# Kernel tuning notes

Measured on AMD Instinct MI355X. Metric: run time of the kernel, lower is better.

The kernel has to match this reference:

```python
import jax, jax.numpy as jnp
import numpy as np

B, Q, HID = 2, 2048, 2048
HQ, HKV, D = 16, 4, 128
EPS = 1e-6
THETA = 1000000.0


def _rmsnorm(x, w):
    # x: [..., D]
    return x * jax.lax.rsqrt(jnp.mean(x * x, axis=-1, keepdims=True) + EPS) * w


def _rope(x, cos, sin):
    # neox-style: split halves. x: [B,Q,H,D], cos/sin: [B,Q,1,D/2]
    d2 = x.shape[-1] // 2
    x1, x2 = x[..., :d2], x[..., d2:]
    return jnp.concatenate([x1 * cos - x2 * sin, x2 * cos + x1 * sin], axis=-1)


def setup_inputs() -> dict:
    key = jax.random.key(0)
    k1, k2, k3 = jax.random.split(key, 3)
    positions = jnp.broadcast_to(jnp.arange(Q, dtype=jnp.int32), (B, Q))
    hidden_states = jax.random.normal(k1, (B, Q, HID), dtype=jnp.float32)
    k_cache = jnp.zeros((B, HKV, Q, D), dtype=jnp.float32)
    v_cache = jnp.zeros((B, HKV, Q, D), dtype=jnp.float32)
    wqkv = jax.random.normal(k2, (HQ * D + 2 * HKV * D, HID), dtype=jnp.float32) * (HID ** -0.5)
    wo = jax.random.normal(k3, (HID, HQ * D), dtype=jnp.float32) * ((HQ * D) ** -0.5)
    q_norm_w = jnp.ones((D,), dtype=jnp.float32)
    k_norm_w = jnp.ones((D,), dtype=jnp.float32)
    return {"positions": positions, "hidden_states": hidden_states, "k_cache": k_cache,
            "v_cache": v_cache, "wqkv": wqkv, "wo": wo, "q_norm_w": q_norm_w,
            "k_norm_w": k_norm_w, "seq_len": Q}


def reference(positions, hidden_states, k_cache, v_cache, wqkv, wo, q_norm_w, k_norm_w, seq_len):
    bsz, qlen, _ = hidden_states.shape
    q_size, kv_size = HQ * D, HKV * D
    scale = D ** -0.5

    qkv = hidden_states.reshape(bsz * qlen, HID) @ wqkv.T  # [B*Q, q+2kv]
    q = qkv[:, :q_size].reshape(bsz, qlen, HQ, D)
    k = qkv[:, q_size:q_size + kv_size].reshape(bsz, qlen, HKV, D)
    v = qkv[:, q_size + kv_size:].reshape(bsz, qlen, HKV, D)

    q = _rmsnorm(q, q_norm_w)
    k = _rmsnorm(k, k_norm_w)

    inv_freq = 1.0 / (THETA ** (jnp.arange(0, D, 2, dtype=jnp.float32) / D))  # [D/2]
    freqs = positions.astype(jnp.float32)[..., None] * inv_freq  # [B,Q,D/2]
    cos = jnp.cos(freqs)[:, :, None, :]
    sin = jnp.sin(freqs)[:, :, None, :]
    q = _rope(q, cos, sin)
    k = _rope(k, cos, sin)

    q = q.transpose(0, 2, 1, 3)  # [B,HQ,Q,D]
    k = k.transpose(0, 2, 1, 3)  # [B,HKV,Q,D]
    v = v.transpose(0, 2, 1, 3)

    start = seq_len - qlen
    k_cache = jax.lax.dynamic_update_slice(k_cache, k, (0, 0, start, 0))
    v_cache = jax.lax.dynamic_update_slice(v_cache, v, (0, 0, start, 0))
    k_full = k_cache[:, :, :seq_len, :]
    v_full = v_cache[:, :, :seq_len, :]

    rep = HQ // HKV
    kf = jnp.repeat(k_full, rep, axis=1)  # [B,HQ,S,D]
    vf = jnp.repeat(v_full, rep, axis=1)

    scores = jnp.einsum('bhqd,bhkd->bhqk', q, kf) * scale
    if qlen == seq_len:  # is_causal path
        causal = jnp.tril(jnp.ones((qlen, seq_len), dtype=bool))
        scores = jnp.where(causal, scores, jnp.finfo(scores.dtype).min)
    attn = jax.nn.softmax(scores, axis=-1)
    out = jnp.einsum('bhqk,bhkd->bhqd', attn, vf)  # [B,HQ,Q,D]
    out = out.transpose(0, 2, 1, 3).reshape(bsz * qlen, HQ * D)
    return (out @ wo.T).reshape(bsz, qlen, HID)
```

## Files before the change

kernel.cpp:

```cpp
#include <hip/hip_runtime.h>

#define B_    2
#define Q_    2048
#define HID_  2048
#define HQ_   16
#define HKV_  4
#define D_    128
#define QSC_  (0.08838834764831843f * 1.4426950408889634f)
#define LOG2_THETA 19.931568569324174f
#define FMAX_ 20.0f

typedef unsigned short u16;
typedef __attribute__((ext_vector_type(8))) short bf16x8;
typedef __attribute__((ext_vector_type(4))) float f32x4;

__device__ __forceinline__ u16 f2bf(float x) {
  union { float f; unsigned int u; } v; v.f = x;
  unsigned int r = v.u + 0x7FFFu + ((v.u >> 16) & 1u);
  return (u16)(r >> 16);
}
__device__ __forceinline__ u16 f2bf_t(float x) {
  union { float f; unsigned int u; } v; v.f = x;
  return (u16)(v.u >> 16);
}

__device__ __forceinline__ void gl2lds16(u16* lds, const u16* g) {
  __builtin_amdgcn_global_load_lds((const __attribute__((address_space(1))) void*)g,
                                   (__attribute__((address_space(3))) void*)lds,
                                   16, 0, 0);
}

#define N4_HID  2097152
#define N4_WQKV 1572864
#define N4_WO   1048576
#define N4_ALL  (N4_HID + N4_WQKV + N4_WO)
#define NROPE   (B_ * Q_ * 64)
__global__ __launch_bounds__(256) void cvt_all(const float* __restrict__ h,
                                               const float* __restrict__ wq,
                                               const float* __restrict__ wo,
                                               const int* __restrict__ pos,
                                               u16* __restrict__ oh,
                                               u16* __restrict__ owq,
                                               u16* __restrict__ owo,
                                               float* __restrict__ rope) {
  int i = blockIdx.x * 256 + threadIdx.x;
  if (i >= N4_ALL) {
    int j = i - N4_ALL;
    int d = j & 63, row = j >> 6;
    float p = (float)pos[row];
    float inv = exp2f(-(float)d * (LOG2_THETA / 64.f));
    float sn, cn;
    sincosf(p * inv, &sn, &cn);
    ((float2*)rope)[j] = make_float2(cn, sn);
    return;
  }
  const float* src; u16* dst; int off;
  if (i < N4_HID)                 { src = h;  dst = oh;  off = i; }
  else if (i < N4_HID + N4_WQKV)  { src = wq; dst = owq; off = i - N4_HID; }
  else                            { src = wo; dst = owo; off = i - N4_HID - N4_WQKV; }
  float4 v = *(const float4*)(src + (size_t)off * 4);
  ushort4 o;
  o.x = f2bf(v.x); o.y = f2bf(v.y); o.z = f2bf(v.z); o.w = f2bf(v.w);
  *(ushort4*)(dst + (size_t)off * 4) = o;
}

__global__ __launch_bounds__(256) void gemm_qkv(const u16* __restrict__ A,
                                                const u16* __restrict__ Bw,
                                                const float* __restrict__ rope,
                                                const float* __restrict__ qw,
                                                const float* __restrict__ kw,
                                                u16* __restrict__ qb,
                                                u16* __restrict__ kb,
                                                u16* __restrict__ vt) {
  __shared__ __align__(16) u16 lds[12288];
  u16* As = lds;
  u16* Bs = lds + 4096;
  const int tid = threadIdx.x;
  const int wv = tid >> 6, lane = tid & 63;
  const int c = lane & 15, quad = lane >> 4;
  const int lr = lane >> 2, lp = lane & 3;
  const int lpg = (lp + 4 - ((lr >> 1) & 3)) & 3;
  const int swq = ((quad + (c >> 1)) & 3) * 8;
  const int m0 = blockIdx.x * 128;
  const int by = blockIdx.y;
  const int n0 = by * 128;
  f32x4 acc[2][8] = {};
  for (int k0 = 0; k0 < HID_; k0 += 32) {
    __syncthreads();
#pragma unroll
    for (int i = 0; i < 2; i++) {
      int r = wv * 16 + i * 64 + lr;
      gl2lds16(As + (size_t)(wv * 64 + i * 256) * 8,
               A + (size_t)(m0 + r) * HID_ + k0 + lpg * 8);
      gl2lds16(Bs + (size_t)(wv * 64 + i * 256) * 8,
               Bw + (size_t)(n0 + r) * HID_ + k0 + lpg * 8);
    }
    __syncthreads();
    bf16x8 af[2], bfr[8];
#pragma unroll
    for (int mi = 0; mi < 2; mi++)
      af[mi] = *(const bf16x8*)(As + (wv * 32 + mi * 16 + c) * 32 + swq);
#pragma unroll
    for (int ni = 0; ni < 8; ni++)
      bfr[ni] = *(const bf16x8*)(Bs + (ni * 16 + c) * 32 + swq);
#pragma unroll
    for (int mi = 0; mi < 2; mi++)
#pragma unroll
      for (int ni = 0; ni < 8; ni++)
        acc[mi][ni] = __builtin_amdgcn_mfma_f32_16x16x32_bf16(af[mi], bfr[ni],
                                                              acc[mi][ni], 0, 0, 0);
  }
  __syncthreads();

  if (by < 20) {
    const bool isq = by < 16;
    const float* w = isq ? qw : kw;
    const float osc = isq ? QSC_ : 1.f;
    float wl[8];
#pragma unroll
    for (int ni = 0; ni < 8; ni++) wl[ni] = w[ni * 16 + c];
    u16* dstbuf = isq ? qb : kb;
    const int hbase = isq ? by : (by - 16);
    const int nheads = isq ? HQ_ : HKV_;
#pragma unroll
    for (int ph = 0; ph < 2; ph++) {
      if (ph) __syncthreads();
      if ((wv >> 1) == ph) {
#pragma unroll
        for (int mi = 0; mi < 2; mi++)
#pragma unroll
          for (int r = 0; r < 4; r++) {
            const int row = m0 + wv * 32 + mi * 16 + quad * 4 + r;
            const int q = row & (Q_ - 1), b = row >> 11;
            float ss = 0.f;
#pragma unroll
            for (int ni = 0; ni < 8; ni++) ss += acc[mi][ni][r] * acc[mi][ni][r];
            ss += __shfl_xor(ss, 1); ss += __shfl_xor(ss, 2);
            ss += __shfl_xor(ss, 4); ss += __shfl_xor(ss, 8);
            const float rn = rsqrtf(ss * (1.f / 128.f) + 1e-6f) * osc;
            u16* lrow = lds + ((wv & 1) * 32 + mi * 16 + quad * 4 + r) * 132;
#pragma unroll
            for (int ni = 0; ni < 4; ni++) {
              float2 cssn = *(const float2*)(rope +
                  ((size_t)(b * Q_ + q) * 64 + ni * 16 + c) * 2);
              float x1 = acc[mi][ni][r]     * wl[ni]     * rn;
              float x2 = acc[mi][ni + 4][r] * wl[ni + 4] * rn;
              lrow[ni * 16 + c]       = f2bf(x1 * cssn.x - x2 * cssn.y);
              lrow[(ni + 4) * 16 + c] = f2bf(x2 * cssn.x + x1 * cssn.y);
            }
          }
      }
      __syncthreads();
      const int rowg = m0 + ph * 64 + (tid >> 2);
      const int q = rowg & (Q_ - 1), b = rowg >> 11;
      u16* dst = dstbuf + (((size_t)(b * nheads) + hbase) * Q_ + q) * D_ + (tid & 3) * 32;
      const u16* srcl = lds + (tid >> 2) * 132 + (tid & 3) * 32;
#pragma unroll
      for (int j = 0; j < 4; j++)
        *(bf16x8*)(dst + j * 8) = *(const bf16x8*)(srcl + j * 8);
    }
  } else {
    const int hk = by - 20;
    const int bb = m0 >> 11, q0 = m0 & (Q_ - 1);
    u16* vw = lds + wv * 3072;
#pragma unroll
    for (int mi = 0; mi < 2; mi++) {
      if (mi) __syncthreads();
#pragma unroll
      for (int ni = 0; ni < 8; ni++) {
        short4 pv;
        pv.x = (short)f2bf(acc[mi][ni][0]); pv.y = (short)f2bf(acc[mi][ni][1]);
        pv.z = (short)f2bf(acc[mi][ni][2]); pv.w = (short)f2bf(acc[mi][ni][3]);
        *(short4*)(vw + (ni * 16 + c) * 24 + quad * 4) = pv;
      }
      __syncthreads();
#pragma unroll
      for (int it = 0; it < 2; it++) {
        const int d = it * 64 + lane;
        const u16* src = vw + d * 24;
        u16* dst = vt + (((size_t)(bb * HKV_) + hk) * D_ + d) * Q_ +
                   q0 + wv * 32 + mi * 16;
        *(bf16x8*)(dst)     = *(const bf16x8*)(src);
        *(bf16x8*)(dst + 8) = *(const bf16x8*)(src + 8);
      }
    }
  }
}

__global__ __launch_bounds__(256) void gemm_bt(const u16* __restrict__ A,
                                               const u16* __restrict__ Bw,
                                               float* __restrict__ C,
                                               int M, int N, int K) {
  __shared__ __align__(16) u16 As[128 * 32];
  __shared__ __align__(16) u16 Bs[128 * 32];
  const int tid = threadIdx.x;
  const int wave = tid >> 6, lane = tid & 63;
  const int wm = wave & 1, wn = wave >> 1;
  const int row16 = lane & 15, quad = lane >> 4;
  const int lr = lane >> 2, lp = lane & 3;
  const int lpg = (lp + 4 - ((lr >> 1) & 3)) & 3;
  const int swq = ((quad + (row16 >> 1)) & 3) * 8;
  const int m0 = blockIdx.x * 128, n0 = blockIdx.y * 128;
  f32x4 acc[4][4] = {};
  for (int k0 = 0; k0 < K; k0 += 32) {
    __syncthreads();
#pragma unroll
    for (int i = 0; i < 2; i++) {
      int r = wave * 16 + i * 64 + lr;
      gl2lds16(As + (size_t)(wave * 64 + i * 256) * 8,
               A + (size_t)(m0 + r) * K + k0 + lpg * 8);
      gl2lds16(Bs + (size_t)(wave * 64 + i * 256) * 8,
               Bw + (size_t)(n0 + r) * K + k0 + lpg * 8);
    }
    __syncthreads();
    bf16x8 af[4], bfr[4];
#pragma unroll
    for (int t = 0; t < 4; t++) {
      af[t]  = *(const bf16x8*)(As + (wm * 64 + t * 16 + row16) * 32 + swq);
      bfr[t] = *(const bf16x8*)(Bs + (wn * 64 + t * 16 + row16) * 32 + swq);
    }
#pragma unroll
    for (int mi = 0; mi < 4; mi++)
#pragma unroll
      for (int ni = 0; ni < 4; ni++)
        acc[mi][ni] = __builtin_amdgcn_mfma_f32_16x16x32_bf16(af[mi], bfr[ni],
                                                              acc[mi][ni], 0, 0, 0);
  }
#pragma unroll
  for (int mi = 0; mi < 4; mi++) {
    int row = m0 + wm * 64 + mi * 16 + quad * 4;
#pragma unroll
    for (int ni = 0; ni < 4; ni++) {
      int col = n0 + wn * 64 + ni * 16 + row16;
#pragma unroll
      for (int r = 0; r < 4; r++)
        C[(size_t)(row + r) * N + col] = acc[mi][ni][r];
    }
  }
}

__global__ __launch_bounds__(256) void attn_fwd(const u16* __restrict__ qb,
                                                const u16* __restrict__ kb,
                                                const u16* __restrict__ vt,
                                                u16* __restrict__ ob) {
  __shared__ __align__(16) u16 lds[8192 + 8192 + 4608];
  u16* Ks = lds;
  u16* Vs = lds + 8192;
  u16* Ps = lds + 16384;
  const int p = blockIdx.x, h = blockIdx.y, b = blockIdx.z;
  const int hk = h >> 2;
  const int tid = threadIdx.x, wave = tid >> 6, lane = tid & 63;
  const int c = lane & 15, quad = lane >> 4;
  const int lr = lane >> 2, lp = lane & 3;
  const int lpg = (lp + 4 - ((lr >> 1) & 3)) & 3;
  const int swq = ((quad + (c >> 1)) & 3) * 8;
  const u16* qg = qb + ((size_t)b * HQ_ + h) * (size_t)Q_ * D_;
  const u16* kg = kb + ((size_t)b * HKV_ + hk) * (size_t)Q_ * D_;
  const u16* vg = vt + ((size_t)b * HKV_ + hk) * (size_t)D_ * Q_;
  u16* Pw = Ps + wave * 1152;
  u16* Bw = Ks + wave * 2176;

#pragma unroll 1
  for (int tp = 0; tp < 2; tp++) {
    const int t = tp ? (31 - p) : p;
    const int q0 = t * 64;
    const int qrow = q0 + wave * 16 + c;
    bf16x8 qf[4];
#pragma unroll
    for (int kk = 0; kk < 4; kk++)
      qf[kk] = *(const bf16x8*)(qg + (size_t)qrow * D_ + kk * 32 + quad * 8);
    f32x4 Oa[8] = {};
    float l_acc = 0.f;

#pragma unroll 1
    for (int kt = 0; kt <= t; kt++) {
      __syncthreads();
#pragma unroll
      for (int i = 0; i < 4; i++) {
        gl2lds16(Ks + (size_t)(i * 256 + wave * 64) * 8,
                 kg + ((size_t)kt * 64 + wave * 16 + lr) * D_ + i * 32 + lpg * 8);
        int d = (i & 1) * 64 + wave * 16 + lr;
        gl2lds16(Vs + (size_t)(i * 256 + wave * 64) * 8,
                 vg + (size_t)d * Q_ + kt * 64 + (i >> 1) * 32 + lpg * 8);
      }
      __syncthreads();
      f32x4 S[4];
#pragma unroll
      for (int n = 0; n < 4; n++) {
        f32x4 a = {-FMAX_, -FMAX_, -FMAX_, -FMAX_};
#pragma unroll
        for (int kk = 0; kk < 4; kk++) {
          bf16x8 kf = *(const bf16x8*)(Ks + kk * 2048 + (n * 16 + c) * 32 + swq);
          a = __builtin_amdgcn_mfma_f32_16x16x32_bf16(kf, qf[kk], a, 0, 0, 0);
        }
        S[n] = a;
      }
      if (kt == t) {
#pragma unroll
        for (int n = 0; n < 4; n++)
#pragma unroll
          for (int r = 0; r < 4; r++) {
            int key = kt * 64 + n * 16 + quad * 4 + r;
            if (key > qrow) S[n][r] = -1e9f;
          }
      }
#pragma unroll
      for (int n = 0; n < 4; n++) {
        float p0 = __builtin_amdgcn_exp2f(S[n][0]);
        float p1 = __builtin_amdgcn_exp2f(S[n][1]);
        float p2 = __builtin_amdgcn_exp2f(S[n][2]);
        float p3 = __builtin_amdgcn_exp2f(S[n][3]);
        l_acc += (p0 + p1) + (p2 + p3);
        short4 pk;
        pk.x = (short)f2bf_t(p0); pk.y = (short)f2bf_t(p1);
        pk.z = (short)f2bf_t(p2); pk.w = (short)f2bf_t(p3);
        *(short4*)(Pw + c * 72 + n * 16 + quad * 4) = pk;
      }
      bf16x8 pf[2];
#pragma unroll
      for (int kk2 = 0; kk2 < 2; kk2++)
        pf[kk2] = *(const bf16x8*)(Pw + c * 72 + kk2 * 32 + quad * 8);
#pragma unroll
      for (int md = 0; md < 8; md++)
#pragma unroll
        for (int kk2 = 0; kk2 < 2; kk2++) {
          bf16x8 vf = *(const bf16x8*)(Vs + kk2 * 4096 + (md * 16 + c) * 32 + swq);
          Oa[md] = __builtin_amdgcn_mfma_f32_16x16x32_bf16(vf, pf[kk2], Oa[md], 0, 0, 0);
        }
    }
    float l_row = l_acc;
    l_row += __shfl_xor(l_row, 16);
    l_row += __shfl_xor(l_row, 32);
    __syncthreads();
    const float invl = 1.f / l_row;
#pragma unroll
    for (int md = 0; md < 8; md++) {
      short4 ok;
      ok.x = (short)f2bf(Oa[md][0] * invl); ok.y = (short)f2bf(Oa[md][1] * invl);
      ok.z = (short)f2bf(Oa[md][2] * invl); ok.w = (short)f2bf(Oa[md][3] * invl);
      *(short4*)(Bw + c * 136 + md * 16 + quad * 4) = ok;
    }
    const int orow = q0 + wave * 16 + lr;
#pragma unroll
    for (int tt = 0; tt < 4; tt++) {
      bf16x8 ov = *(const bf16x8*)(Bw + lr * 136 + lp * 32 + tt * 8);
      *(bf16x8*)(ob + ((size_t)(b * Q_ + orow) * HQ_ + h) * D_ + lp * 32 + tt * 8) = ov;
    }
  }
}

extern "C" void kernel_launch(void* const* d_in, const int* in_sizes, int n_in,
                              void* d_out, int out_size, void* d_ws, size_t ws_size,
                              hipStream_t stream) {
  const int*   positions = (const int*)  d_in[0];
  const float* hidden    = (const float*)d_in[1];
  const float* wqkv      = (const float*)d_in[4];
  const float* wo        = (const float*)d_in[5];
  const float* qnw       = (const float*)d_in[6];
  const float* knw       = (const float*)d_in[7];
  char* ws = (char*)d_ws;
  u16*   hid_bf  = (u16*)(ws);
  u16*   wqkv_bf = (u16*)(ws + 16777216);
  u16*   wo_bf   = (u16*)(ws + 29360128);
  u16*   q_bf    = (u16*)(ws + 37748736);
  u16*   k_bf    = (u16*)(ws + 54525952);
  u16*   vt_bf   = (u16*)(ws + 58720256);
  float* rope    = (float*)(ws + 62914560);
  u16*   attn_bf = hid_bf;

  cvt_all<<<19456, 256, 0, stream>>>(hidden, wqkv, wo, positions,
                                     hid_bf, wqkv_bf, wo_bf, rope);
  gemm_qkv<<<dim3(32, 24), 256, 0, stream>>>(hid_bf, wqkv_bf, rope, qnw, knw,
                                             q_bf, k_bf, vt_bf);
  attn_fwd<<<dim3(16, 16, 2), 256, 0, stream>>>(q_bf, k_bf, vt_bf, attn_bf);
  gemm_bt<<<dim3(32, 16), 256, 0, stream>>>(attn_bf, wo_bf, (float*)d_out, 4096, 2048, 2048);
}
```

Baseline: 336.9 us.

## Use 2x2 wave tiling in QKV GEMM with permuted weight rows for RoPE

```diff
diff --git a/kernel.cpp b/kernel.cpp
--- a/kernel.cpp
+++ b/kernel.cpp
@@ -54,14 +54,32 @@
     ((float2*)rope)[j] = make_float2(cn, sn);
     return;
   }
-  const float* src; u16* dst; int off;
-  if (i < N4_HID)                 { src = h;  dst = oh;  off = i; }
-  else if (i < N4_HID + N4_WQKV)  { src = wq; dst = owq; off = i - N4_HID; }
-  else                            { src = wo; dst = owo; off = i - N4_HID - N4_WQKV; }
-  float4 v = *(const float4*)(src + (size_t)off * 4);
-  ushort4 o;
-  o.x = f2bf(v.x); o.y = f2bf(v.y); o.z = f2bf(v.z); o.w = f2bf(v.w);
-  *(ushort4*)(dst + (size_t)off * 4) = o;
+  if (i < N4_HID) {
+    float4 v = *(const float4*)(h + (size_t)i * 4);
+    ushort4 o;
+    o.x = f2bf(v.x); o.y = f2bf(v.y); o.z = f2bf(v.z); o.w = f2bf(v.w);
+    *(ushort4*)(oh + (size_t)i * 4) = o;
+  } else if (i < N4_HID + N4_WQKV) {
+    int off = i - N4_HID;
+    float4 v = *(const float4*)(wq + (size_t)off * 4);
+    int row = off >> 9;
+    int dst_row = row;
+    if (row < 2560) {
+      int d = row & 127;
+      int j = (d & 31) | ((d >> 1) & 32) | ((d & 32) << 1);
+      dst_row = (row & ~127) | j;
+    }
+    size_t doff = ((size_t)dst_row << 9) | (off & 511);
+    ushort4 o;
+    o.x = f2bf(v.x); o.y = f2bf(v.y); o.z = f2bf(v.z); o.w = f2bf(v.w);
+    *(ushort4*)(owq + doff * 4) = o;
+  } else {
+    int off = i - N4_HID - N4_WQKV;
+    float4 v = *(const float4*)(wo + (size_t)off * 4);
+    ushort4 o;
+    o.x = f2bf(v.x); o.y = f2bf(v.y); o.z = f2bf(v.z); o.w = f2bf(v.w);
+    *(ushort4*)(owo + (size_t)off * 4) = o;
+  }
 }
 
 __global__ __launch_bounds__(256) void gemm_qkv(const u16* __restrict__ A,
@@ -77,6 +95,7 @@
   u16* Bs = lds + 4096;
   const int tid = threadIdx.x;
   const int wv = tid >> 6, lane = tid & 63;
+  const int wm = wv & 1, wn = wv >> 1;
   const int c = lane & 15, quad = lane >> 4;
   const int lr = lane >> 2, lp = lane & 3;
   const int lpg = (lp + 4 - ((lr >> 1) & 3)) & 3;
@@ -84,7 +103,7 @@
   const int m0 = blockIdx.x * 128;
   const int by = blockIdx.y;
   const int n0 = by * 128;
-  f32x4 acc[2][8] = {};
+  f32x4 acc[4][4] = {};
   for (int k0 = 0; k0 < HID_; k0 += 32) {
     __syncthreads();
 #pragma unroll
@@ -96,17 +115,16 @@
                Bw + (size_t)(n0 + r) * HID_ + k0 + lpg * 8);
     }
     __syncthreads();
-    bf16x8 af[2], bfr[8];
-#pragma unroll
-    for (int mi = 0; mi < 2; mi++)
-      af[mi] = *(const bf16x8*)(As + (wv * 32 + mi * 16 + c) * 32 + swq);
-#pragma unroll
-    for (int ni = 0; ni < 8; ni++)
-      bfr[ni] = *(const bf16x8*)(Bs + (ni * 16 + c) * 32 + swq);
-#pragma unroll
-    for (int mi = 0; mi < 2; mi++)
-#pragma unroll
-      for (int ni = 0; ni < 8; ni++)
+    bf16x8 af[4], bfr[4];
+#pragma unroll
+    for (int t = 0; t < 4; t++) {
+      af[t]  = *(const bf16x8*)(As + (wm * 64 + t * 16 + c) * 32 + swq);
+      bfr[t] = *(const bf16x8*)(Bs + (wn * 64 + t * 16 + c) * 32 + swq);
+    }
+#pragma unroll
+    for (int mi = 0; mi < 4; mi++)
+#pragma unroll
+      for (int ni = 0; ni < 4; ni++)
         acc[mi][ni] = __builtin_amdgcn_mfma_f32_16x16x32_bf16(af[mi], bfr[ni],
                                                               acc[mi][ni], 0, 0, 0);
   }
@@ -116,37 +134,65 @@
     const bool isq = by < 16;
     const float* w = isq ? qw : kw;
     const float osc = isq ? QSC_ : 1.f;
-    float wl[8];
-#pragma unroll
-    for (int ni = 0; ni < 8; ni++) wl[ni] = w[ni * 16 + c];
+    float ssp[4][4];
+#pragma unroll
+    for (int mi = 0; mi < 4; mi++)
+#pragma unroll
+      for (int r = 0; r < 4; r++) {
+        float s = 0.f;
+#pragma unroll
+        for (int ni = 0; ni < 4; ni++) s += acc[mi][ni][r] * acc[mi][ni][r];
+        s += __shfl_xor(s, 1); s += __shfl_xor(s, 2);
+        s += __shfl_xor(s, 4); s += __shfl_xor(s, 8);
+        ssp[mi][r] = s;
+      }
+    float* fss = (float*)(lds + 8704);
+    if (c == 0) {
+#pragma unroll
+      for (int mi = 0; mi < 4; mi++)
+#pragma unroll
+        for (int r = 0; r < 4; r++)
+          fss[(wm * 64 + mi * 16 + quad * 4 + r) * 2 + wn] = ssp[mi][r];
+    }
+    __syncthreads();
+    float rn[4][4];
+#pragma unroll
+    for (int mi = 0; mi < 4; mi++)
+#pragma unroll
+      for (int r = 0; r < 4; r++) {
+        float2 both = ((const float2*)fss)[wm * 64 + mi * 16 + quad * 4 + r];
+        rn[mi][r] = rsqrtf((both.x + both.y) * (1.f / 128.f) + 1e-6f) * osc;
+      }
+    float w1[2], w2[2];
+#pragma unroll
+    for (int pn = 0; pn < 2; pn++) {
+      w1[pn] = w[wn * 32 + pn * 16 + c];
+      w2[pn] = w[64 + wn * 32 + pn * 16 + c];
+    }
     u16* dstbuf = isq ? qb : kb;
     const int hbase = isq ? by : (by - 16);
     const int nheads = isq ? HQ_ : HKV_;
 #pragma unroll
     for (int ph = 0; ph < 2; ph++) {
       if (ph) __syncthreads();
-      if ((wv >> 1) == ph) {
-#pragma unroll
-        for (int mi = 0; mi < 2; mi++)
+      if (wm == ph) {
+#pragma unroll
+        for (int mi = 0; mi < 4; mi++)
 #pragma unroll
           for (int r = 0; r < 4; r++) {
-            const int row = m0 + wv * 32 + mi * 16 + quad * 4 + r;
-            const int q = row & (Q_ - 1), b = row >> 11;
-            float ss = 0.f;
-#pragma unroll
-            for (int ni = 0; ni < 8; ni++) ss += acc[mi][ni][r] * acc[mi][ni][r];
-            ss += __shfl_xor(ss, 1); ss += __shfl_xor(ss, 2);
-            ss += __shfl_xor(ss, 4); ss += __shfl_xor(ss, 8);
-            const float rn = rsqrtf(ss * (1.f / 128.f) + 1e-6f) * osc;
-            u16* lrow = lds + ((wv & 1) * 32 + mi * 16 + quad * 4 + r) * 132;
-#pragma unroll
-            for (int ni = 0; ni < 4; ni++) {
-              float2 cssn = *(const float2*)(rope +
-                  ((size_t)(b * Q_ + q) * 64 + ni * 16 + c) * 2);
-              float x1 = acc[mi][ni][r]     * wl[ni]     * rn;
-              float x2 = acc[mi][ni + 4][r] * wl[ni + 4] * rn;
-              lrow[ni * 16 + c]       = f2bf(x1 * cssn.x - x2 * cssn.y);
-              lrow[(ni + 4) * 16 + c] = f2bf(x2 * cssn.x + x1 * cssn.y);
+            const int rl = mi * 16 + quad * 4 + r;
+            const int rowg = m0 + ph * 64 + rl;
+            const int q = rowg & (Q_ - 1), b = rowg >> 11;
+            const float* rp = rope + ((size_t)(b * Q_ + q) * 64) * 2;
+            u16* lrow = lds + rl * 132;
+#pragma unroll
+            for (int pn = 0; pn < 2; pn++) {
+              const int d1 = wn * 32 + pn * 16 + c;
+              float2 cs = *(const float2*)(rp + d1 * 2);
+              float x1 = acc[mi][pn][r]     * w1[pn] * rn[mi][r];
+              float x2 = acc[mi][pn + 2][r] * w2[pn] * rn[mi][r];
+              lrow[d1]      = f2bf(x1 * cs.x - x2 * cs.y);
+              lrow[d1 + 64] = f2bf(x2 * cs.x + x1 * cs.y);
             }
           }
       }
@@ -162,27 +208,28 @@
   } else {
     const int hk = by - 20;
     const int bb = m0 >> 11, q0 = m0 & (Q_ - 1);
-    u16* vw = lds + wv * 3072;
-#pragma unroll
-    for (int mi = 0; mi < 2; mi++) {
-      if (mi) __syncthreads();
-#pragma unroll
-      for (int ni = 0; ni < 8; ni++) {
-        short4 pv;
-        pv.x = (short)f2bf(acc[mi][ni][0]); pv.y = (short)f2bf(acc[mi][ni][1]);
-        pv.z = (short)f2bf(acc[mi][ni][2]); pv.w = (short)f2bf(acc[mi][ni][3]);
-        *(short4*)(vw + (ni * 16 + c) * 24 + quad * 4) = pv;
+#pragma unroll
+    for (int ph = 0; ph < 2; ph++) {
+      if (ph) __syncthreads();
+      if (wn == ph) {
+#pragma unroll
+        for (int mi = 0; mi < 4; mi++)
+#pragma unroll
+          for (int ni = 0; ni < 4; ni++) {
+            short4 pv;
+            pv.x = (short)f2bf(acc[mi][ni][0]); pv.y = (short)f2bf(acc[mi][ni][1]);
+            pv.z = (short)f2bf(acc[mi][ni][2]); pv.w = (short)f2bf(acc[mi][ni][3]);
+            *(short4*)(lds + (ni * 16 + c) * 132 + wm * 64 + mi * 16 + quad * 4) = pv;
+          }
       }
       __syncthreads();
-#pragma unroll
-      for (int it = 0; it < 2; it++) {
-        const int d = it * 64 + lane;
-        const u16* src = vw + d * 24;
-        u16* dst = vt + (((size_t)(bb * HKV_) + hk) * D_ + d) * Q_ +
-                   q0 + wv * 32 + mi * 16;
-        *(bf16x8*)(dst)     = *(const bf16x8*)(src);
-        *(bf16x8*)(dst + 8) = *(const bf16x8*)(src + 8);
-      }
+      const int dl = tid >> 2;
+      u16* dst = vt + (((size_t)(bb * HKV_) + hk) * D_ + ph * 64 + dl) * Q_ +
+                 q0 + (tid & 3) * 32;
+      const u16* srcl = lds + dl * 132 + (tid & 3) * 32;
+#pragma unroll
+      for (int j = 0; j < 4; j++)
+        *(bf16x8*)(dst + j * 8) = *(const bf16x8*)(srcl + j * 8);
     }
   }
 }
```

After: 375.6 us. 1.12x slower.
